# Optimization experiments

Measured on AMD Instinct MI355X. Metric: run time of the kernel, lower is better.

The kernel has to match this reference:

```python
import jax, jax.numpy as jnp
import numpy as np

N_NODES = 40000
N_EDGES = 640000
IN_CH = 128
HID1, HID2 = 512, 256
OUT_CH = 2
NUM_GRAPHS = 16
EPS = 1e-5


def layer_norm(x, g, b):
    mu = jnp.mean(x, axis=-1, keepdims=True)
    var = jnp.mean(jnp.square(x - mu), axis=-1, keepdims=True)
    return (x - mu) * jax.lax.rsqrt(var + EPS) * g + b


def gcn_conv(x, src, dst, ew, W, b, n_nodes):
    # PyG GCNConv: x' = x @ W; symmetric normalization with self-loops already
    # appended to (src, dst, ew) by the caller; bias added after aggregation.
    xw = x @ W                                            # [N, out]
    deg = jax.ops.segment_sum(ew, dst, num_segments=n_nodes)
    dinv = jnp.where(deg > 0, jax.lax.rsqrt(deg), 0.0)    # deg^{-1/2}, 0 for isolated
    norm = dinv[src] * ew * dinv[dst]                     # [E+N]
    msgs = norm[:, None] * xw[src]                        # gather + scale
    out = jax.ops.segment_sum(msgs, dst, num_segments=n_nodes)
    return out + b


def setup_inputs() -> dict:
    key = jax.random.key(0)
    ks = jax.random.split(key, 12)
    x = jax.random.normal(ks[0], (N_NODES, IN_CH), dtype=jnp.float32)
    edge_index = jax.random.randint(ks[1], (2, N_EDGES), 0, N_NODES, dtype=jnp.int64)
    edge_weight = jax.random.uniform(ks[2], (N_EDGES,), dtype=jnp.float32)
    batch = jnp.sort(jax.random.randint(ks[3], (N_NODES,), 0, NUM_GRAPHS, dtype=jnp.int64))
    # parameters (Glorot-ish scale)
    W1 = jax.random.normal(ks[4], (IN_CH, HID1), dtype=jnp.float32) / np.sqrt(IN_CH)
    b1 = jnp.zeros((HID1,), dtype=jnp.float32)
    g1 = jnp.ones((HID1,), dtype=jnp.float32)
    be1 = jnp.zeros((HID1,), dtype=jnp.float32)
    W2 = jax.random.normal(ks[5], (HID1, HID2), dtype=jnp.float32) / np.sqrt(HID1)
    b2 = jnp.zeros((HID2,), dtype=jnp.float32)
    g2 = jnp.ones((HID2,), dtype=jnp.float32)
    be2 = jnp.zeros((HID2,), dtype=jnp.float32)
    Wfc = jax.random.normal(ks[6], (HID2, OUT_CH), dtype=jnp.float32) / np.sqrt(HID2)
    bfc = jnp.zeros((OUT_CH,), dtype=jnp.float32)
    return {"x": x, "edge_index": edge_index, "edge_weight": edge_weight,
            "batch": batch, "W1": W1, "b1": b1, "g1": g1, "be1": be1,
            "W2": W2, "b2": b2, "g2": g2, "be2": be2, "Wfc": Wfc, "bfc": bfc}


def reference(x, edge_index, edge_weight, batch, W1, b1, g1, be1, W2, b2, g2, be2, Wfc, bfc):
    n = x.shape[0]
    loop = jnp.arange(n, dtype=edge_index.dtype)
    src = jnp.concatenate([edge_index[0], loop])
    dst = jnp.concatenate([edge_index[1], loop])
    ew = jnp.concatenate([edge_weight, jnp.ones((n,), dtype=edge_weight.dtype)])

    h = gcn_conv(x, src, dst, ew, W1, b1, n)
    h = layer_norm(jax.nn.relu(h), g1, be1)          # dropout = identity (eval)
    h3 = gcn_conv(h, src, dst, ew, W2, b2, n)
    h3 = layer_norm(jax.nn.relu(h3), g2, be2)

    # global mean pool over graph ids
    sums = jax.ops.segment_sum(h3, batch, num_segments=NUM_GRAPHS)
    cnts = jax.ops.segment_sum(jnp.ones((n,), dtype=h3.dtype), batch, num_segments=NUM_GRAPHS)
    pooled = sums / jnp.maximum(cnts, 1.0)[:, None]
    out = pooled @ Wfc + bfc
    return h3, out
```

## Files before the change

### kernel.cpp

```cpp
#include <hip/hip_runtime.h>
#include <hip/hip_bf16.h>

#define N_NODES   40000
#define N_EDGES   640000
#define IN_CH     128
#define HID1      512
#define HID2      256
#define OUT_CH    2
#define NUM_GRAPHS 16
#define EPSF      1e-5f
#define SCAN_NB   157
#define FIXSC     1048576.0f

typedef unsigned short u16;
typedef unsigned int   u32;
typedef unsigned long long u64;
using short8 = __attribute__((ext_vector_type(8))) short;
using f32x4  = __attribute__((ext_vector_type(4))) float;

__device__ __forceinline__ float b2f(u16 u) {
    return __uint_as_float(((u32)u) << 16);
}
__device__ __forceinline__ u16 f2b(float f) {
    u32 u = __float_as_uint(f);
    u32 r = (u + 0x7FFFu + ((u >> 16) & 1u)) >> 16;
    return (u16)r;
}
__device__ __forceinline__ void gload_lds16(const u16* g, u16* l) {
    __builtin_amdgcn_global_load_lds((const __attribute__((address_space(1))) u32*)g,
                                     (__attribute__((address_space(3))) u32*)l, 16, 0, 0);
}

__global__ __launch_bounds__(256) void pack_kernel(const int* __restrict__ dst,
                                                   const float* __restrict__ ew,
                                                   u64* __restrict__ packed,
                                                   int* __restrict__ eoff) {
    int t = blockIdx.x * blockDim.x + threadIdx.x;
    if (t >= N_EDGES) return;
    int d = dst[t];
    u64 inc = (1ull << 40) | (u64)__float2uint_rn(ew[t] * FIXSC);
    u64 old = atomicAdd(&packed[d], inc);
    eoff[t] = (int)(old >> 40);
}

__global__ __launch_bounds__(256) void scan_p1_kernel(const u64* __restrict__ packed,
                                                      float* __restrict__ dinv,
                                                      int* __restrict__ rowptr,
                                                      int* __restrict__ blocksum) {
    __shared__ int sd[256];
    const int t = threadIdx.x;
    const int i = blockIdx.x * 256 + t;
    int v = 0;
    if (i < N_NODES) {
        u64 p = packed[i];
        v = (int)(p >> 40);
        float deg = (float)(p & ((1ull << 40) - 1)) * (1.0f / FIXSC);
        dinv[i] = rsqrtf(deg + 1.0f);
    }
    sd[t] = v;
    __syncthreads();
    for (int off = 1; off < 256; off <<= 1) {
        int u = (t >= off) ? sd[t - off] : 0;
        __syncthreads();
        sd[t] += u;
        __syncthreads();
    }
    if (i < N_NODES) rowptr[i] = sd[t] - v;
    if (t == 255) blocksum[blockIdx.x] = sd[255];
}

__global__ __launch_bounds__(256) void scan_p2_kernel(int* __restrict__ blocksum,
                                                      int* __restrict__ bprefix) {
    __shared__ int sd[256];
    const int t = threadIdx.x;
    const int v = (t < SCAN_NB) ? blocksum[t] : 0;
    sd[t] = v;
    __syncthreads();
    for (int off = 1; off < 256; off <<= 1) {
        int u = (t >= off) ? sd[t - off] : 0;
        __syncthreads();
        sd[t] += u;
        __syncthreads();
    }
    bprefix[t] = sd[t] - v;
}

__global__ __launch_bounds__(256) void scan_p3_kernel(int* __restrict__ rowptr,
                                                      const int* __restrict__ bprefix) {
    const int i = blockIdx.x * 256 + threadIdx.x;
    if (i < N_NODES) rowptr[i] += bprefix[blockIdx.x];
    if (i == 0) rowptr[N_NODES] = N_EDGES;
}

__global__ __launch_bounds__(256) void scatter_kernel(const int* __restrict__ src,
                                                      const int* __restrict__ dst,
                                                      const float* __restrict__ ew,
                                                      const float* __restrict__ dinv,
                                                      const int* __restrict__ rowptr,
                                                      const int* __restrict__ eoff,
                                                      int2* __restrict__ csr_pair) {
    int t = blockIdx.x * blockDim.x + threadIdx.x;
    if (t >= N_EDGES) return;
    int s = src[t], d = dst[t];
    int pos = rowptr[d] + eoff[t];
    float norm = dinv[s] * ew[t] * dinv[d];
    int2 pr; pr.x = s; pr.y = __float_as_int(norm);
    csr_pair[pos] = pr;
}

__global__ __launch_bounds__(256) void cast_x_kernel(const float* __restrict__ x,
                                                     u16* __restrict__ xb) {
    int t = blockIdx.x * blockDim.x + threadIdx.x;
    if (t < N_NODES * IN_CH / 4) {
        float4 v = ((const float4*)x)[t];
        ushort4 o = { f2b(v.x), f2b(v.y), f2b(v.z), f2b(v.w) };
        ((ushort4*)xb)[t] = o;
    }
}

__global__ __launch_bounds__(256) void transpose_cast_kernel(const float* __restrict__ W,
                                                             u16* __restrict__ WT,
                                                             int R, int Ccols) {
    int idx = blockIdx.x * blockDim.x + threadIdx.x;
    if (idx >= R * Ccols) return;
    int r = idx / Ccols, c = idx % Ccols;
    WT[(size_t)c * R + r] = f2b(W[idx]);
}

__global__ __launch_bounds__(256) void agg128_kernel(const int* __restrict__ rowptr,
                                                     const int2* __restrict__ csr_pair,
                                                     const float* __restrict__ dinv,
                                                     const u16* __restrict__ xb,
                                                     u16* __restrict__ outb) {
    const int node = (blockIdx.x * blockDim.x + threadIdx.x) >> 6;
    const int lane = threadIdx.x & 63;
    if (node >= N_NODES) return;
    const float ds = dinv[node];
    const float wself = ds * ds;
    const int e0 = rowptr[node], e1 = rowptr[node + 1];
    const int c0 = lane * 2;

    ushort2 v = *(const ushort2*)&xb[(size_t)node * IN_CH + c0];
    float ax = wself * b2f(v.x), ay = wself * b2f(v.y);
    int e = e0;
    for (; e + 8 <= e1; e += 8) {
        int2 pi[8]; ushort2 ui[8];
#pragma unroll
        for (int j = 0; j < 8; ++j) pi[j] = csr_pair[e + j];
#pragma unroll
        for (int j = 0; j < 8; ++j) ui[j] = *(const ushort2*)&xb[(size_t)pi[j].x * IN_CH + c0];
#pragma unroll
        for (int j = 0; j < 8; ++j) {
            float w = __int_as_float(pi[j].y);
            ax += w * b2f(ui[j].x);
            ay += w * b2f(ui[j].y);
        }
    }
    for (; e < e1; ++e) {
        int2 p = csr_pair[e];
        float w = __int_as_float(p.y);
        ushort2 u = *(const ushort2*)&xb[(size_t)p.x * IN_CH + c0];
        ax += w * b2f(u.x);
        ay += w * b2f(u.y);
    }
    ushort2 o = { f2b(ax), f2b(ay) };
    *(ushort2*)&outb[(size_t)node * IN_CH + c0] = o;
}

__global__ __launch_bounds__(256) void agg256_ln_kernel(const int* __restrict__ rowptr,
                                                        const int2* __restrict__ csr_pair,
                                                        const float* __restrict__ dinv,
                                                        const u16* __restrict__ hwb,
                                                        const float* __restrict__ bias,
                                                        const float* __restrict__ g,
                                                        const float* __restrict__ be,
                                                        float* __restrict__ out) {
    const int node = (blockIdx.x * blockDim.x + threadIdx.x) >> 6;
    const int lane = threadIdx.x & 63;
    if (node >= N_NODES) return;
    const float ds = dinv[node];
    const float wself = ds * ds;
    const int e0 = rowptr[node], e1 = rowptr[node + 1];
    const int c0 = lane * 4;

    ushort4 v = *(const ushort4*)&hwb[(size_t)node * HID2 + c0];
    float4 acc = { wself * b2f(v.x), wself * b2f(v.y), wself * b2f(v.z), wself * b2f(v.w) };
    int e = e0;
    for (; e + 8 <= e1; e += 8) {
        int2 pi[8]; ushort4 ui[8];
#pragma unroll
        for (int j = 0; j < 8; ++j) pi[j] = csr_pair[e + j];
#pragma unroll
        for (int j = 0; j < 8; ++j) ui[j] = *(const ushort4*)&hwb[(size_t)pi[j].x * HID2 + c0];
#pragma unroll
        for (int j = 0; j < 8; ++j) {
            float w = __int_as_float(pi[j].y);
            acc.x += w * b2f(ui[j].x);
            acc.y += w * b2f(ui[j].y);
            acc.z += w * b2f(ui[j].z);
            acc.w += w * b2f(ui[j].w);
        }
    }
    for (; e < e1; ++e) {
        int2 p = csr_pair[e];
        float w = __int_as_float(p.y);
        ushort4 u = *(const ushort4*)&hwb[(size_t)p.x * HID2 + c0];
        acc.x += w * b2f(u.x);
        acc.y += w * b2f(u.y);
        acc.z += w * b2f(u.z);
        acc.w += w * b2f(u.w);
    }
    float vv[4];
    float sum = 0.f, sq = 0.f;
#pragma unroll
    for (int j = 0; j < 4; ++j) {
        float xv = ((const float*)&acc)[j] + bias[c0 + j];
        xv = fmaxf(xv, 0.f);
        vv[j] = xv;
        sum += xv;
        sq += xv * xv;
    }
#pragma unroll
    for (int off = 32; off >= 1; off >>= 1) {
        sum += __shfl_xor(sum, off);
        sq  += __shfl_xor(sq, off);
    }
    const float mean = sum * (1.0f / HID2);
    const float var = sq * (1.0f / HID2) - mean * mean;
    const float r = rsqrtf(var + EPSF);
    float4 o;
    o.x = (vv[0] - mean) * r * g[c0 + 0] + be[c0 + 0];
    o.y = (vv[1] - mean) * r * g[c0 + 1] + be[c0 + 1];
    o.z = (vv[2] - mean) * r * g[c0 + 2] + be[c0 + 2];
    o.w = (vv[3] - mean) * r * g[c0 + 3] + be[c0 + 3];
    *(float4*)&out[(size_t)node * HID2 + c0] = o;
}

template <int K, int N, int ASTRIDE>
__global__ __launch_bounds__(256) void mfma_gemm128(const u16* __restrict__ A,
                                                    const u16* __restrict__ BT,
                                                    u16* __restrict__ Cb) {
    __shared__ u16 As[128 * 32];
    __shared__ u16 Bs[128 * 32];
    const int t = threadIdx.x;
    const int rowbase = blockIdx.x * 128;
    const int colbase = blockIdx.y * 128;
    const int l = t & 63;
    const int wv = t >> 6;
    const int wm = (wv >> 1) * 64;
    const int wn = (wv & 1) * 64;
    const int fr = l & 15;
    const int fg = l >> 4;

    f32x4 acc[4][4];
#pragma unroll
    for (int a = 0; a < 4; ++a)
#pragma unroll
        for (int b = 0; b < 4; ++b)
            acc[a][b] = (f32x4){0.f, 0.f, 0.f, 0.f};

    const int c0i = wv * 128 + l;
    const int c1i = c0i + 64;
    int ar0 = rowbase + (c0i >> 2); if (ar0 >= N_NODES) ar0 = N_NODES - 1;
    int ar1 = rowbase + (c1i >> 2); if (ar1 >= N_NODES) ar1 = N_NODES - 1;
    const u16* ag0 = A + (size_t)ar0 * ASTRIDE + (c0i & 3) * 8;
    const u16* ag1 = A + (size_t)ar1 * ASTRIDE + (c1i & 3) * 8;
    const u16* bg0 = BT + (size_t)(colbase + (c0i >> 2)) * K + (c0i & 3) * 8;
    const u16* bg1 = BT + (size_t)(colbase + (c1i >> 2)) * K + (c1i & 3) * 8;
    u16* al0 = As + c0i * 8;
    u16* al1 = As + c1i * 8;
    u16* bl0 = Bs + c0i * 8;
    u16* bl1 = Bs + c1i * 8;

    for (int k0 = 0; k0 < K; k0 += 32) {
        gload_lds16(ag0 + k0, al0);
        gload_lds16(ag1 + k0, al1);
        gload_lds16(bg0 + k0, bl0);
        gload_lds16(bg1 + k0, bl1);
        __syncthreads();

        short8 af[4], bf[4];
#pragma unroll
        for (int fm = 0; fm < 4; ++fm)
            af[fm] = *(const short8*)&As[(wm + fm * 16 + fr) * 32 + fg * 8];
#pragma unroll
        for (int fn = 0; fn < 4; ++fn)
            bf[fn] = *(const short8*)&Bs[(wn + fn * 16 + fr) * 32 + fg * 8];
#pragma unroll
        for (int fm = 0; fm < 4; ++fm)
#pragma unroll
            for (int fn = 0; fn < 4; ++fn)
                acc[fm][fn] = __builtin_amdgcn_mfma_f32_16x16x32_bf16(af[fm], bf[fn], acc[fm][fn], 0, 0, 0);
        __syncthreads();
    }

#pragma unroll
    for (int fm = 0; fm < 4; ++fm)
#pragma unroll
        for (int fn = 0; fn < 4; ++fn) {
#pragma unroll
            for (int i = 0; i < 4; ++i) {
                int row = rowbase + wm + fm * 16 + fg * 4 + i;
                if (row < N_NODES) {
                    int col = colbase + wn + fn * 16 + fr;
                    Cb[(size_t)row * N + col] = f2b(acc[fm][fn][i]);
                }
            }
        }
}

__global__ __launch_bounds__(256) void relu_ln512b_kernel(u16* __restrict__ io,
                                                          const float* __restrict__ bias,
                                                          const float* __restrict__ g,
                                                          const float* __restrict__ be) {
    const int wv = (blockIdx.x * blockDim.x + threadIdx.x) >> 6;
    const int lane = threadIdx.x & 63;
    if (wv >= N_NODES) return;
    u16* __restrict__ row = io + (size_t)wv * HID1;
    const int c0 = lane * 8;
    short8 raw = *(const short8*)&row[c0];
    float v[8];
    float sum = 0.f, sq = 0.f;
#pragma unroll
    for (int j = 0; j < 8; ++j) {
        float xv = b2f((u16)raw[j]) + bias[c0 + j];
        xv = fmaxf(xv, 0.f);
        v[j] = xv;
        sum += xv;
        sq += xv * xv;
    }
#pragma unroll
    for (int off = 32; off >= 1; off >>= 1) {
        sum += __shfl_xor(sum, off);
        sq  += __shfl_xor(sq, off);
    }
    const float mean = sum * (1.0f / HID1);
    const float var = sq * (1.0f / HID1) - mean * mean;
    const float r = rsqrtf(var + EPSF);
    short8 o;
#pragma unroll
    for (int j = 0; j < 8; ++j)
        o[j] = (short)f2b((v[j] - mean) * r * g[c0 + j] + be[c0 + j]);
    *(short8*)&row[c0] = o;
}

__global__ __launch_bounds__(64) void bounds_kernel(const int* __restrict__ batch,
                                                    int* __restrict__ gstart) {
    int g = threadIdx.x;
    if (g > NUM_GRAPHS) return;
    int lo = 0, hi = N_NODES;
    while (lo < hi) {
        int mid = (lo + hi) >> 1;
        if (batch[mid] < g) lo = mid + 1; else hi = mid;
    }
    gstart[g] = lo;
}

__global__ __launch_bounds__(256) void pool2_kernel(const float* __restrict__ h3,
                                                    const int* __restrict__ gstart,
                                                    float* __restrict__ pooled) {
    const int g = blockIdx.x, chunk = blockIdx.y;
    const int s = gstart[g], e = gstart[g + 1];
    const int len = e - s;
    const int c0 = s + (len * chunk) / 16;
    const int c1 = s + (len * (chunk + 1)) / 16;
    float acc = 0.f;
    for (int n = c0; n < c1; ++n)
        acc += h3[(size_t)n * HID2 + threadIdx.x];
    atomicAdd(&pooled[g * HID2 + threadIdx.x], acc);
}

__global__ __launch_bounds__(64) void fc_kernel(const float* __restrict__ pooled,
                                                const int* __restrict__ gstart,
                                                const float* __restrict__ Wfc,
                                                const float* __restrict__ bfc,
                                                float* __restrict__ out) {
    const int t = threadIdx.x;
    if (t >= NUM_GRAPHS * OUT_CH) return;
    const int g = t >> 1;
    const int o = t & 1;
    const int len = gstart[g + 1] - gstart[g];
    const float inv = 1.0f / fmaxf((float)len, 1.0f);
    float s = 0.f;
    for (int k = 0; k < HID2; ++k)
        s += pooled[g * HID2 + k] * Wfc[k * OUT_CH + o];
    out[t] = s * inv + bfc[o];
}

extern "C" void kernel_launch(void* const* d_in, const int* in_sizes, int n_in,
                              void* d_out, int out_size, void* d_ws, size_t ws_size,
                              hipStream_t stream) {
    const float* x   = (const float*)d_in[0];
    const int*   ei  = (const int*)d_in[1];
    const float* ew  = (const float*)d_in[2];
    const int*   bat = (const int*)d_in[3];
    const float* W1  = (const float*)d_in[4];
    const float* b1  = (const float*)d_in[5];
    const float* g1  = (const float*)d_in[6];
    const float* be1 = (const float*)d_in[7];
    const float* W2  = (const float*)d_in[8];
    const float* b2  = (const float*)d_in[9];
    const float* g2  = (const float*)d_in[10];
    const float* be2 = (const float*)d_in[11];
    const float* Wfc = (const float*)d_in[12];
    const float* bfc = (const float*)d_in[13];

    const int* srcArr = ei;
    const int* dstArr = ei + N_EDGES;

    float* out = (float*)d_out;
    float* h3  = out;
    float* fcO = out + (size_t)N_NODES * HID2;

    float* ws       = (float*)d_ws;
    u64*   packed   = (u64*)ws;
    float* dinv     = ws + 81920;
    int*   rowptr   = (int*)(ws + 122880);
    int*   gstart   = (int*)(ws + 163968);
    int*   blocksum = (int*)(ws + 164032);
    int*   bprefix  = (int*)(ws + 164288);
    int*   eoff     = (int*)(ws + 164544);
    int2*  csr_pair = (int2*)(ws + 804544);
    u16*   xb       = (u16*)(ws + 2084544);
    u16*   agg1b    = (u16*)(ws + 4644544);
    u16*   hb       = (u16*)(ws + 7204544);
    u16*   hwb      = (u16*)(ws + 17444544);
    u16*   W1T      = (u16*)(ws + 22564544);
    u16*   W2T      = (u16*)(ws + 22597312);
    float* pooled   = ws + 22662848;

    hipMemsetAsync(packed, 0, 40960 * sizeof(u64), stream);
    pack_kernel<<<(N_EDGES + 255) / 256, 256, 0, stream>>>(dstArr, ew, packed, eoff);
    scan_p1_kernel<<<SCAN_NB, 256, 0, stream>>>(packed, dinv, rowptr, blocksum);
    scan_p2_kernel<<<1, 256, 0, stream>>>(blocksum, bprefix);
    scan_p3_kernel<<<SCAN_NB, 256, 0, stream>>>(rowptr, bprefix);
    scatter_kernel<<<(N_EDGES + 255) / 256, 256, 0, stream>>>(
        srcArr, dstArr, ew, dinv, rowptr, eoff, csr_pair);

    cast_x_kernel<<<(N_NODES * IN_CH / 4 + 255) / 256, 256, 0, stream>>>(x, xb);
    transpose_cast_kernel<<<(IN_CH * HID1 + 255) / 256, 256, 0, stream>>>(W1, W1T, IN_CH, HID1);
    transpose_cast_kernel<<<(HID1 * HID2 + 255) / 256, 256, 0, stream>>>(W2, W2T, HID1, HID2);

    agg128_kernel<<<(N_NODES + 3) / 4, 256, 0, stream>>>(
        rowptr, csr_pair, dinv, xb, agg1b);
    {
        dim3 grid((N_NODES + 127) / 128, HID1 / 128);
        mfma_gemm128<IN_CH, HID1, IN_CH><<<grid, 256, 0, stream>>>(agg1b, W1T, hb);
    }
    relu_ln512b_kernel<<<(N_NODES + 3) / 4, 256, 0, stream>>>(hb, b1, g1, be1);

    {
        dim3 grid((N_NODES + 127) / 128, HID2 / 128);
        mfma_gemm128<HID1, HID2, HID1><<<grid, 256, 0, stream>>>(hb, W2T, hwb);
    }
    agg256_ln_kernel<<<(N_NODES + 3) / 4, 256, 0, stream>>>(
        rowptr, csr_pair, dinv, hwb, b2, g2, be2, h3);

    bounds_kernel<<<1, 64, 0, stream>>>(bat, gstart);
    hipMemsetAsync(pooled, 0, NUM_GRAPHS * HID2 * sizeof(float), stream);
    {
        dim3 grid(NUM_GRAPHS, 16);
        pool2_kernel<<<grid, 256, 0, stream>>>(h3, gstart, pooled);
    }
    fc_kernel<<<1, 64, 0, stream>>>(pooled, gstart, Wfc, bfc, fcO);
}
```

Measured before the change: 264.1 us.

## Fuse GEMM1 with ReLU+LayerNorm, split-edge aggregation, merge small prep kernels

Several changes land together. A new 64-row by 512-column MFMA GEMM kernel applies bias, ReLU and LayerNorm in its epilogue, so the separate LN pass and its read-back of the bf16 hidden buffer go away. Both aggregation kernels now let each half-wavefront handle alternate edges with wider per-lane loads, then combine the halves with a cross-half shuffle. The x-cast and both weight transposes become one prep kernel, and the graph-bounds search moves into the scan kernel. Pooling writes per-chunk partial sums that the fc kernel reduces, replacing the memset and atomics. The fused GEMM uses a large LDS tile (32 KB for B alone) and 512-thread blocks, which may lower occupancy.

```diff
diff --git a/kernel.cpp b/kernel.cpp
--- a/kernel.cpp
+++ b/kernel.cpp
@@ -70,7 +70,9 @@
 }
 
 __global__ __launch_bounds__(256) void scan_p2_kernel(int* __restrict__ blocksum,
-                                                      int* __restrict__ bprefix) {
+                                                      int* __restrict__ bprefix,
+                                                      const int* __restrict__ batch,
+                                                      int* __restrict__ gstart) {
     __shared__ int sd[256];
     const int t = threadIdx.x;
     const int v = (t < SCAN_NB) ? blocksum[t] : 0;
@@ -83,6 +85,14 @@
         __syncthreads();
     }
     bprefix[t] = sd[t] - v;
+    if (t <= NUM_GRAPHS) {
+        int lo = 0, hi = N_NODES;
+        while (lo < hi) {
+            int mid = (lo + hi) >> 1;
+            if (batch[mid] < t) lo = mid + 1; else hi = mid;
+        }
+        gstart[t] = lo;
+    }
 }
 
 __global__ __launch_bounds__(256) void scan_p3_kernel(int* __restrict__ rowptr,
@@ -108,23 +118,26 @@
     csr_pair[pos] = pr;
 }
 
-__global__ __launch_bounds__(256) void cast_x_kernel(const float* __restrict__ x,
-                                                     u16* __restrict__ xb) {
+__global__ __launch_bounds__(256) void prep_kernel(const float* __restrict__ x,
+                                                   u16* __restrict__ xb,
+                                                   const float* __restrict__ W1,
+                                                   u16* __restrict__ W1T,
+                                                   const float* __restrict__ W2,
+                                                   u16* __restrict__ W2T) {
     int t = blockIdx.x * blockDim.x + threadIdx.x;
     if (t < N_NODES * IN_CH / 4) {
         float4 v = ((const float4*)x)[t];
         ushort4 o = { f2b(v.x), f2b(v.y), f2b(v.z), f2b(v.w) };
         ((ushort4*)xb)[t] = o;
     }
-}
-
-__global__ __launch_bounds__(256) void transpose_cast_kernel(const float* __restrict__ W,
-                                                             u16* __restrict__ WT,
-                                                             int R, int Ccols) {
-    int idx = blockIdx.x * blockDim.x + threadIdx.x;
-    if (idx >= R * Ccols) return;
-    int r = idx / Ccols, c = idx % Ccols;
-    WT[(size_t)c * R + r] = f2b(W[idx]);
+    if (t < IN_CH * HID1) {
+        int r = t / HID1, c = t % HID1;
+        W1T[(size_t)c * IN_CH + r] = f2b(W1[t]);
+    }
+    if (t < HID1 * HID2) {
+        int r = t / HID2, c = t % HID2;
+        W2T[(size_t)c * HID1 + r] = f2b(W2[t]);
+    }
 }
 
 __global__ __launch_bounds__(256) void agg128_kernel(const int* __restrict__ rowptr,
@@ -133,38 +146,48 @@
                                                      const u16* __restrict__ xb,
                                                      u16* __restrict__ outb) {
     const int node = (blockIdx.x * blockDim.x + threadIdx.x) >> 6;
-    const int lane = threadIdx.x & 63;
+    const int l = threadIdx.x & 63;
     if (node >= N_NODES) return;
+    const int half = l >> 5, cl = l & 31;
     const float ds = dinv[node];
-    const float wself = ds * ds;
+    const float wself = half ? 0.f : ds * ds;
     const int e0 = rowptr[node], e1 = rowptr[node + 1];
-    const int c0 = lane * 2;
-
-    ushort2 v = *(const ushort2*)&xb[(size_t)node * IN_CH + c0];
-    float ax = wself * b2f(v.x), ay = wself * b2f(v.y);
+    const int c0 = cl * 4;
+
+    ushort4 sv = *(const ushort4*)&xb[(size_t)node * IN_CH + c0];
+    float acc[4] = { wself * b2f(sv.x), wself * b2f(sv.y),
+                     wself * b2f(sv.z), wself * b2f(sv.w) };
     int e = e0;
     for (; e + 8 <= e1; e += 8) {
-        int2 pi[8]; ushort2 ui[8];
-#pragma unroll
-        for (int j = 0; j < 8; ++j) pi[j] = csr_pair[e + j];
-#pragma unroll
-        for (int j = 0; j < 8; ++j) ui[j] = *(const ushort2*)&xb[(size_t)pi[j].x * IN_CH + c0];
-#pragma unroll
-        for (int j = 0; j < 8; ++j) {
-            float w = __int_as_float(pi[j].y);
-            ax += w * b2f(ui[j].x);
-            ay += w * b2f(ui[j].y);
-        }
-    }
-    for (; e < e1; ++e) {
-        int2 p = csr_pair[e];
+        int2 p[4]; ushort4 u[4];
+#pragma unroll
+        for (int j = 0; j < 4; ++j) p[j] = csr_pair[e + half + 2 * j];
+#pragma unroll
+        for (int j = 0; j < 4; ++j) u[j] = *(const ushort4*)&xb[(size_t)p[j].x * IN_CH + c0];
+#pragma unroll
+        for (int j = 0; j < 4; ++j) {
+            float w = __int_as_float(p[j].y);
+            acc[0] += w * b2f(u[j].x);
+            acc[1] += w * b2f(u[j].y);
+            acc[2] += w * b2f(u[j].z);
+            acc[3] += w * b2f(u[j].w);
+        }
+    }
+    for (int ee = e + half; ee < e1; ee += 2) {
+        int2 p = csr_pair[ee];
         float w = __int_as_float(p.y);
-        ushort2 u = *(const ushort2*)&xb[(size_t)p.x * IN_CH + c0];
-        ax += w * b2f(u.x);
-        ay += w * b2f(u.y);
-    }
-    ushort2 o = { f2b(ax), f2b(ay) };
-    *(ushort2*)&outb[(size_t)node * IN_CH + c0] = o;
+        ushort4 u = *(const ushort4*)&xb[(size_t)p.x * IN_CH + c0];
+        acc[0] += w * b2f(u.x);
+        acc[1] += w * b2f(u.y);
+        acc[2] += w * b2f(u.z);
+        acc[3] += w * b2f(u.w);
+    }
+#pragma unroll
+    for (int j = 0; j < 4; ++j) acc[j] += __shfl_xor(acc[j], 32);
+    float a0 = half ? acc[2] : acc[0];
+    float a1 = half ? acc[3] : acc[1];
+    ushort2 o = { f2b(a0), f2b(a1) };
+    *(ushort2*)&outb[(size_t)node * IN_CH + c0 + half * 2] = o;
 }
 
 __global__ __launch_bounds__(256) void agg256_ln_kernel(const int* __restrict__ rowptr,
@@ -176,64 +199,198 @@
                                                         const float* __restrict__ be,
                                                         float* __restrict__ out) {
     const int node = (blockIdx.x * blockDim.x + threadIdx.x) >> 6;
-    const int lane = threadIdx.x & 63;
+    const int l = threadIdx.x & 63;
     if (node >= N_NODES) return;
+    const int half = l >> 5, cl = l & 31;
     const float ds = dinv[node];
-    const float wself = ds * ds;
+    const float wself = half ? 0.f : ds * ds;
     const int e0 = rowptr[node], e1 = rowptr[node + 1];
-    const int c0 = lane * 4;
-
-    ushort4 v = *(const ushort4*)&hwb[(size_t)node * HID2 + c0];
-    float4 acc = { wself * b2f(v.x), wself * b2f(v.y), wself * b2f(v.z), wself * b2f(v.w) };
+    const int c0 = cl * 8;
+
+    short8 sv = *(const short8*)&hwb[(size_t)node * HID2 + c0];
+    float acc[8];
+#pragma unroll
+    for (int j = 0; j < 8; ++j) acc[j] = wself * b2f((u16)sv[j]);
+
     int e = e0;
     for (; e + 8 <= e1; e += 8) {
-        int2 pi[8]; ushort4 ui[8];
-#pragma unroll
-        for (int j = 0; j < 8; ++j) pi[j] = csr_pair[e + j];
-#pragma unroll
-        for (int j = 0; j < 8; ++j) ui[j] = *(const ushort4*)&hwb[(size_t)pi[j].x * HID2 + c0];
-#pragma unroll
-        for (int j = 0; j < 8; ++j) {
-            float w = __int_as_float(pi[j].y);
-            acc.x += w * b2f(ui[j].x);
-            acc.y += w * b2f(ui[j].y);
-            acc.z += w * b2f(ui[j].z);
-            acc.w += w * b2f(ui[j].w);
-        }
-    }
-    for (; e < e1; ++e) {
-        int2 p = csr_pair[e];
+        int2 p[4]; short8 u[4];
+#pragma unroll
+        for (int j = 0; j < 4; ++j) p[j] = csr_pair[e + half + 2 * j];
+#pragma unroll
+        for (int j = 0; j < 4; ++j) u[j] = *(const short8*)&hwb[(size_t)p[j].x * HID2 + c0];
+#pragma unroll
+        for (int j = 0; j < 4; ++j) {
+            float w = __int_as_float(p[j].y);
+#pragma unroll
+            for (int k = 0; k < 8; ++k) acc[k] += w * b2f((u16)u[j][k]);
+        }
+    }
+    for (int ee = e + half; ee < e1; ee += 2) {
+        int2 p = csr_pair[ee];
         float w = __int_as_float(p.y);
-        ushort4 u = *(const ushort4*)&hwb[(size_t)p.x * HID2 + c0];
-        acc.x += w * b2f(u.x);
-        acc.y += w * b2f(u.y);
-        acc.z += w * b2f(u.z);
-        acc.w += w * b2f(u.w);
-    }
-    float vv[4];
+        short8 u = *(const short8*)&hwb[(size_t)p.x * HID2 + c0];
+#pragma unroll
+        for (int k = 0; k < 8; ++k) acc[k] += w * b2f((u16)u[k]);
+    }
+#pragma unroll
+    for (int j = 0; j < 8; ++j) acc[j] += __shfl_xor(acc[j], 32);
+
+    float4 blo = *(const float4*)&bias[c0];
+    float4 bhi = *(const float4*)&bias[c0 + 4];
+    float vv[8];
     float sum = 0.f, sq = 0.f;
 #pragma unroll
-    for (int j = 0; j < 4; ++j) {
-        float xv = ((const float*)&acc)[j] + bias[c0 + j];
-        xv = fmaxf(xv, 0.f);
+    for (int j = 0; j < 8; ++j) {
+        float bj = (j < 4) ? ((const float*)&blo)[j] : ((const float*)&bhi)[j - 4];
+        float xv = fmaxf(acc[j] + bj, 0.f);
         vv[j] = xv;
         sum += xv;
         sq += xv * xv;
     }
 #pragma unroll
-    for (int off = 32; off >= 1; off >>= 1) {
+    for (int off = 1; off <= 16; off <<= 1) {
         sum += __shfl_xor(sum, off);
         sq  += __shfl_xor(sq, off);
     }
     const float mean = sum * (1.0f / HID2);
     const float var = sq * (1.0f / HID2) - mean * mean;
     const float r = rsqrtf(var + EPSF);
+
+    const int cw = c0 + half * 4;
+    float4 gq = *(const float4*)&g[cw];
+    float4 bq = *(const float4*)&be[cw];
+    float s0 = half ? vv[4] : vv[0];
+    float s1 = half ? vv[5] : vv[1];
+    float s2 = half ? vv[6] : vv[2];
+    float s3 = half ? vv[7] : vv[3];
     float4 o;
-    o.x = (vv[0] - mean) * r * g[c0 + 0] + be[c0 + 0];
-    o.y = (vv[1] - mean) * r * g[c0 + 1] + be[c0 + 1];
-    o.z = (vv[2] - mean) * r * g[c0 + 2] + be[c0 + 2];
-    o.w = (vv[3] - mean) * r * g[c0 + 3] + be[c0 + 3];
-    *(float4*)&out[(size_t)node * HID2 + c0] = o;
+    o.x = (s0 - mean) * r * gq.x + bq.x;
+    o.y = (s1 - mean) * r * gq.y + bq.y;
+    o.z = (s2 - mean) * r * gq.z + bq.z;
+    o.w = (s3 - mean) * r * gq.w + bq.w;
+    *(float4*)&out[(size_t)node * HID2 + cw] = o;
+}
+
+__global__ __launch_bounds__(512) void gemm1ln_kernel(const u16* __restrict__ A,
+                                                      const u16* __restrict__ BT,
+                                                      const float* __restrict__ b1,
+                                                      const float* __restrict__ g1,
+                                                      const float* __restrict__ be1,
+                                                      u16* __restrict__ H) {
+    __shared__ u16 As[64 * 32];
+    __shared__ u16 Bs[512 * 32];
+    __shared__ float lsum[8][64];
+    __shared__ float lsq[8][64];
+    __shared__ float lmean[64];
+    __shared__ float lrstd[64];
+    const int t = threadIdx.x;
+    const int l = t & 63;
+    const int wv = t >> 6;
+    const int fr = l & 15;
+    const int fg = l >> 4;
+    const int rowbase = blockIdx.x * 64;
+
+    f32x4 acc[4][4];
+#pragma unroll
+    for (int a = 0; a < 4; ++a)
+#pragma unroll
+        for (int b = 0; b < 4; ++b)
+            acc[a][b] = (f32x4){0.f, 0.f, 0.f, 0.f};
+
+    for (int k0 = 0; k0 < IN_CH; k0 += 32) {
+        if (t < 256)
+            gload_lds16(A + (size_t)(rowbase + (t >> 2)) * IN_CH + k0 + (t & 3) * 8,
+                        As + t * 8);
+#pragma unroll
+        for (int j = 0; j < 4; ++j) {
+            int c = t + 512 * j;
+            gload_lds16(BT + (size_t)(c >> 2) * IN_CH + k0 + (c & 3) * 8,
+                        Bs + c * 8);
+        }
+        __syncthreads();
+
+        short8 af[4], bf[4];
+#pragma unroll
+        for (int fm = 0; fm < 4; ++fm)
+            af[fm] = *(const short8*)&As[(fm * 16 + fr) * 32 + fg * 8];
+#pragma unroll
+        for (int fn = 0; fn < 4; ++fn)
+            bf[fn] = *(const short8*)&Bs[(wv * 64 + fn * 16 + fr) * 32 + fg * 8];
+#pragma unroll
+        for (int fm = 0; fm < 4; ++fm)
+#pragma unroll
+            for (int fn = 0; fn < 4; ++fn)
+                acc[fm][fn] = __builtin_amdgcn_mfma_f32_16x16x32_bf16(af[fm], bf[fn], acc[fm][fn], 0, 0, 0);
+        __syncthreads();
+    }
+
+    const int colb = wv * 64;
+    float bc[4], gc[4], bec[4];
+#pragma unroll
+    for (int fn = 0; fn < 4; ++fn) {
+        int col = colb + fn * 16 + fr;
+        bc[fn] = b1[col];
+        gc[fn] = g1[col];
+        bec[fn] = be1[col];
+    }
+    float ps[4][4], pq[4][4];
+#pragma unroll
+    for (int fm = 0; fm < 4; ++fm)
+#pragma unroll
+        for (int i = 0; i < 4; ++i) { ps[fm][i] = 0.f; pq[fm][i] = 0.f; }
+#pragma unroll
+    for (int fm = 0; fm < 4; ++fm)
+#pragma unroll
+        for (int fn = 0; fn < 4; ++fn)
+#pragma unroll
+            for (int i = 0; i < 4; ++i) {
+                float xv = fmaxf(acc[fm][fn][i] + bc[fn], 0.f);
+                acc[fm][fn][i] = xv;
+                ps[fm][i] += xv;
+                pq[fm][i] += xv * xv;
+            }
+#pragma unroll
+    for (int off = 1; off < 16; off <<= 1)
+#pragma unroll
+        for (int fm = 0; fm < 4; ++fm)
+#pragma unroll
+            for (int i = 0; i < 4; ++i) {
+                ps[fm][i] += __shfl_xor(ps[fm][i], off);
+                pq[fm][i] += __shfl_xor(pq[fm][i], off);
+            }
+    if (fr == 0) {
+#pragma unroll
+        for (int fm = 0; fm < 4; ++fm)
+#pragma unroll
+            for (int i = 0; i < 4; ++i) {
+                int row = fm * 16 + fg * 4 + i;
+                lsum[wv][row] = ps[fm][i];
+                lsq[wv][row] = pq[fm][i];
+            }
+    }
+    __syncthreads();
+    if (t < 64) {
+        float s = 0.f, q = 0.f;
+#pragma unroll
+        for (int w = 0; w < 8; ++w) { s += lsum[w][t]; q += lsq[w][t]; }
+        float mean = s * (1.0f / HID1);
+        float var = q * (1.0f / HID1) - mean * mean;
+        lmean[t] = mean;
+        lrstd[t] = rsqrtf(var + EPSF);
+    }
+    __syncthreads();
+#pragma unroll
+    for (int fm = 0; fm < 4; ++fm)
+#pragma unroll
+        for (int fn = 0; fn < 4; ++fn)
+#pragma unroll
+            for (int i = 0; i < 4; ++i) {
+                int row = fm * 16 + fg * 4 + i;
+                int col = colb + fn * 16 + fr;
+                float o = (acc[fm][fn][i] - lmean[row]) * lrstd[row] * gc[fn] + bec[fn];
+                H[(size_t)(rowbase + row) * HID1 + col] = f2b(o);
+            }
 }
 
 template <int K, int N, int ASTRIDE>
@@ -309,56 +466,9 @@
         }
 }
 
-__global__ __launch_bounds__(256) void relu_ln512b_kernel(u16* __restrict__ io,
-                                                          const float* __restrict__ bias,
-                                                          const float* __restrict__ g,
-                                                          const float* __restrict__ be) {
-    const int wv = (blockIdx.x * blockDim.x + threadIdx.x) >> 6;
-    const int lane = threadIdx.x & 63;
-    if (wv >= N_NODES) return;
-    u16* __restrict__ row = io + (size_t)wv * HID1;
-    const int c0 = lane * 8;
-    short8 raw = *(const short8*)&row[c0];
-    float v[8];
-    float sum = 0.f, sq = 0.f;
-#pragma unroll
-    for (int j = 0; j < 8; ++j) {
-        float xv = b2f((u16)raw[j]) + bias[c0 + j];
-        xv = fmaxf(xv, 0.f);
-        v[j] = xv;
-        sum += xv;
-        sq += xv * xv;
-    }
-#pragma unroll
-    for (int off = 32; off >= 1; off >>= 1) {
-        sum += __shfl_xor(sum, off);
-        sq  += __shfl_xor(sq, off);
-    }
-    const float mean = sum * (1.0f / HID1);
-    const float var = sq * (1.0f / HID1) - mean * mean;
-    const float r = rsqrtf(var + EPSF);
-    short8 o;
-#pragma unroll
-    for (int j = 0; j < 8; ++j)
-        o[j] = (short)f2b((v[j] - mean) * r * g[c0 + j] + be[c0 + j]);
-    *(short8*)&row[c0] = o;
-}
-
-__global__ __launch_bounds__(64) void bounds_kernel(const int* __restrict__ batch,
-                                                    int* __restrict__ gstart) {
-    int g = threadIdx.x;
-    if (g > NUM_GRAPHS) return;
-    int lo = 0, hi = N_NODES;
-    while (lo < hi) {
-        int mid = (lo + hi) >> 1;
-        if (batch[mid] < g) lo = mid + 1; else hi = mid;
-    }
-    gstart[g] = lo;
-}
-
 __global__ __launch_bounds__(256) void pool2_kernel(const float* __restrict__ h3,
                                                     const int* __restrict__ gstart,
-                                                    float* __restrict__ pooled) {
+                                                    float* __restrict__ part) {
     const int g = blockIdx.x, chunk = blockIdx.y;
     const int s = gstart[g], e = gstart[g + 1];
     const int len = e - s;
@@ -367,24 +477,36 @@
     float acc = 0.f;
     for (int n = c0; n < c1; ++n)
         acc += h3[(size_t)n * HID2 + threadIdx.x];
-    atomicAdd(&pooled[g * HID2 + threadIdx.x], acc);
-}
-
-__global__ __launch_bounds__(64) void fc_kernel(const float* __restrict__ pooled,
-                                                const int* __restrict__ gstart,
-                                                const float* __restrict__ Wfc,
-                                                const float* __restrict__ bfc,
-                                                float* __restrict__ out) {
+    part[(size_t)(g * 16 + chunk) * HID2 + threadIdx.x] = acc;
+}
+
+__global__ __launch_bounds__(256) void fc_kernel(const float* __restrict__ part,
+                                                 const int* __restrict__ gstart,
+                                                 const float* __restrict__ Wfc,
+                                                 const float* __restrict__ bfc,
+                                                 float* __restrict__ out) {
+    __shared__ float r0[256], r1[256];
     const int t = threadIdx.x;
-    if (t >= NUM_GRAPHS * OUT_CH) return;
-    const int g = t >> 1;
-    const int o = t & 1;
-    const int len = gstart[g + 1] - gstart[g];
-    const float inv = 1.0f / fmaxf((float)len, 1.0f);
-    float s = 0.f;
-    for (int k = 0; k < HID2; ++k)
-        s += pooled[g * HID2 + k] * Wfc[k * OUT_CH + o];
-    out[t] = s * inv + bfc[o];
+    const float w0 = Wfc[t * 2], w1 = Wfc[t * 2 + 1];
+    for (int g = 0; g < NUM_GRAPHS; ++g) {
+        float v = 0.f;
+#pragma unroll
+        for (int k = 0; k < 16; ++k)
+            v += part[(size_t)(g * 16 + k) * HID2 + t];
+        r0[t] = v * w0;
+        r1[t] = v * w1;
+        __syncthreads();
+        for (int off = 128; off >= 1; off >>= 1) {
+            if (t < off) { r0[t] += r0[t + off]; r1[t] += r1[t + off]; }
+            __syncthreads();
+        }
+        if (t == 0) {
+            float inv = 1.0f / fmaxf((float)(gstart[g + 1] - gstart[g]), 1.0f);
+            out[g * 2 + 0] = r0[0] * inv + bfc[0];
+            out[g * 2 + 1] = r1[0] * inv + bfc[1];
+        }
+        __syncthreads();
+    }
 }
 
 extern "C" void kernel_launch(void* const* d_in, const int* in_sizes, int n_in,
@@ -427,27 +549,22 @@
     u16*   hwb      = (u16*)(ws + 17444544);
     u16*   W1T      = (u16*)(ws + 22564544);
     u16*   W2T      = (u16*)(ws + 22597312);
-    float* pooled   = ws + 22662848;
+    float* part     = ws + 22662848;
 
     hipMemsetAsync(packed, 0, 40960 * sizeof(u64), stream);
     pack_kernel<<<(N_EDGES + 255) / 256, 256, 0, stream>>>(dstArr, ew, packed, eoff);
     scan_p1_kernel<<<SCAN_NB, 256, 0, stream>>>(packed, dinv, rowptr, blocksum);
-    scan_p2_kernel<<<1, 256, 0, stream>>>(blocksum, bprefix);
+    scan_p2_kernel<<<1, 256, 0, stream>>>(blocksum, bprefix, bat, gstart);
     scan_p3_kernel<<<SCAN_NB, 256, 0, stream>>>(rowptr, bprefix);
     scatter_kernel<<<(N_EDGES + 255) / 256, 256, 0, stream>>>(
         srcArr, dstArr, ew, dinv, rowptr, eoff, csr_pair);
 
-    cast_x_kernel<<<(N_NODES * IN_CH / 4 + 255) / 256, 256, 0, stream>>>(x, xb);
-    transpose_cast_kernel<<<(IN_CH * HID1 + 255) / 256, 256, 0, stream>>>(W1, W1T, IN_CH, HID1);
-    transpose_cast_kernel<<<(HID1 * HID2 + 255) / 256, 256, 0, stream>>>(W2, W2T, HID1, HID2);
+    prep_kernel<<<(N_NODES * IN_CH / 4 + 255) / 256, 256, 0, stream>>>(
+        x, xb, W1, W1T, W2, W2T);
 
     agg128_kernel<<<(N_NODES + 3) / 4, 256, 0, stream>>>(
         rowptr, csr_pair, dinv, xb, agg1b);
-    {
-        dim3 grid((N_NODES + 127) / 128, HID1 / 128);
-        mfma_gemm128<IN_CH, HID1, IN_CH><<<grid, 256, 0, stream>>>(agg1b, W1T, hb);
-    }
-    relu_ln512b_kernel<<<(N_NODES + 3) / 4, 256, 0, stream>>>(hb, b1, g1, be1);
+    gemm1ln_kernel<<<N_NODES / 64, 512, 0, stream>>>(agg1b, W1T, b1, g1, be1, hb);
 
     {
         dim3 grid((N_NODES + 127) / 128, HID2 / 128);
@@ -456,11 +573,9 @@
     agg256_ln_kernel<<<(N_NODES + 3) / 4, 256, 0, stream>>>(
         rowptr, csr_pair, dinv, hwb, b2, g2, be2, h3);
 
-    bounds_kernel<<<1, 64, 0, stream>>>(bat, gstart);
-    hipMemsetAsync(pooled, 0, NUM_GRAPHS * HID2 * sizeof(float), stream);
     {
         dim3 grid(NUM_GRAPHS, 16);
-        pool2_kernel<<<grid, 256, 0, stream>>>(h3, gstart, pooled);
-    }
-    fc_kernel<<<1, 64, 0, stream>>>(pooled, gstart, Wfc, bfc, fcO);
-}
+        pool2_kernel<<<grid, 256, 0, stream>>>(h3, gstart, part);
+    }
+    fc_kernel<<<1, 256, 0, stream>>>(part, gstart, Wfc, bfc, fcO);
+}
```

Result: no change. 261.5 us (-1.0%).
